# Performance work log

Hardware: AMD Instinct MI355X
Metric: run time of the kernel (lower is better)

Reference implementation:

```python
import jax, jax.numpy as jnp
import numpy as np
from jax.ops import segment_sum

NUM_GRAPHS = 1024

def setup_inputs() -> dict:
    key = jax.random.key(0)
    ks = jax.random.split(key, 10)
    N, E = 100000, 6400000
    x = jax.random.normal(ks[0], (N, 3), dtype=jnp.float32)
    edge_index = jax.random.randint(ks[1], (2, E), 0, N, dtype=jnp.int64)
    batch = jnp.sort(jax.random.randint(ks[2], (N,), 0, NUM_GRAPHS, dtype=jnp.int64))
    # GCNConv weights (glorot-ish scale) and biases
    W1 = jax.random.normal(ks[3], (3, 16), dtype=jnp.float32) * (1.0 / np.sqrt(3))
    b1 = jnp.zeros((16,), dtype=jnp.float32)
    W2 = jax.random.normal(ks[4], (16, 32), dtype=jnp.float32) * (1.0 / np.sqrt(16))
    b2 = jnp.zeros((32,), dtype=jnp.float32)
    Wl = jax.random.normal(ks[5], (32, 3), dtype=jnp.float32) * (1.0 / np.sqrt(32))
    bl = jnp.zeros((3,), dtype=jnp.float32)
    return {"x": x, "edge_index": edge_index, "batch": batch,
            "W1": W1, "b1": b1, "W2": W2, "b2": b2, "Wl": Wl, "bl": bl}

def _gcn_conv(x, src, dst, norm, W, b, num_nodes):
    # h = X W ; out[dst] += norm * h[src]  (symmetric-normalized scatter-add)
    h = x @ W                                    # [N, F_out]
    msg = h[src] * norm[:, None]                 # [E+N, F_out]
    out = segment_sum(msg, dst, num_segments=num_nodes)
    return out + b

def reference(x, edge_index, batch, W1, b1, W2, b2, Wl, bl):
    N = x.shape[0]
    # add self-loops (PyG GCNConv default)
    loops = jnp.arange(N, dtype=edge_index.dtype)
    src = jnp.concatenate([edge_index[0], loops])
    dst = jnp.concatenate([edge_index[1], loops])
    # symmetric normalization: deg over destination, norm = d^-1/2[src] * d^-1/2[dst]
    deg = segment_sum(jnp.ones_like(dst, dtype=x.dtype), dst, num_segments=N)
    dinv = jnp.where(deg > 0, jax.lax.rsqrt(deg), 0.0)
    norm = dinv[src] * dinv[dst]
    h = jax.nn.relu(_gcn_conv(x, src, dst, norm, W1, b1, N))
    h = jax.nn.relu(_gcn_conv(h, src, dst, norm, W2, b2, N))
    # global mean pool over graphs
    sums = segment_sum(h, batch, num_segments=NUM_GRAPHS)          # [G, 32]
    cnts = segment_sum(jnp.ones((N,), dtype=h.dtype), batch, num_segments=NUM_GRAPHS)
    pooled = sums / jnp.maximum(cnts, 1.0)[:, None]
    return pooled @ Wl + bl
```

## Files before the change

### kernel.cpp

```cpp
#include <hip/hip_runtime.h>
#include <hip/hip_fp16.h>

#define NG 1024
#define SCAN_B 1024
#define BSH2 9
#define GN 512
#define MAXBIN 256
#define NB2 256
#define SCB 1024
#define TSZ 8192
#define TS2 8192
#define PGR 64

__global__ void k_scanA(const int* __restrict__ in, int* __restrict__ tmp,
                        int* __restrict__ part, int L) {
    __shared__ int s[SCAN_B];
    int gid = blockIdx.x * SCAN_B + threadIdx.x;
    s[threadIdx.x] = (gid < L) ? in[gid] : 0;
    __syncthreads();
    for (int off = 1; off < SCAN_B; off <<= 1) {
        int t = (threadIdx.x >= off) ? s[threadIdx.x - off] : 0;
        __syncthreads();
        s[threadIdx.x] += t;
        __syncthreads();
    }
    if (gid < L) tmp[gid] = s[threadIdx.x];
    if (threadIdx.x == SCAN_B - 1) part[blockIdx.x] = s[SCAN_B - 1];
}

__global__ void k_scanB(int* __restrict__ part, int NB) {
    __shared__ int s[SCAN_B];
    int v = (threadIdx.x < NB) ? part[threadIdx.x] : 0;
    s[threadIdx.x] = v;
    __syncthreads();
    for (int off = 1; off < SCAN_B; off <<= 1) {
        int t = (threadIdx.x >= off) ? s[threadIdx.x - off] : 0;
        __syncthreads();
        s[threadIdx.x] += t;
        __syncthreads();
    }
    if (threadIdx.x < NB) part[threadIdx.x] = threadIdx.x ? s[threadIdx.x - 1] : 0;
}

__global__ void k_applyT(const int* __restrict__ tmp2, const int* __restrict__ part2,
                         int* __restrict__ histT, int L,
                         float* __restrict__ pooled, float* __restrict__ cnt) {
    int k = blockIdx.x * blockDim.x + threadIdx.x;
    if (k < L) {
        int incl = tmp2[k] + part2[k >> 10];
        int orig = histT[k];
        histT[k] = incl - orig;
        if (k == L - 1) histT[L] = incl;
    }
    if (k < NG * 32) pooled[k] = 0.0f;
    if (k < NG) cnt[k] = 0.0f;
}

__global__ __launch_bounds__(SCB) void k_hist(const int* __restrict__ dst,
                                              int* __restrict__ histT,
                                              int E, int CH, int NBIN) {
    __shared__ int cnt_s[MAXBIN];
    if (threadIdx.x < MAXBIN) cnt_s[threadIdx.x] = 0;
    __syncthreads();
    int blk = blockIdx.x;
    int s0 = blk * CH, s1 = s0 + CH; if (s1 > E) s1 = E;
    for (int e = s0 + threadIdx.x; e < s1; e += SCB)
        atomicAdd(&cnt_s[dst[e] >> BSH2], 1);
    __syncthreads();
    for (int b = threadIdx.x; b < NBIN; b += SCB)
        histT[b * NB2 + blk] = cnt_s[b];
}

__global__ __launch_bounds__(1024) void k_scatter(const int* __restrict__ src,
                                                  const int* __restrict__ dst,
                                                  const int* __restrict__ offT,
                                                  unsigned* __restrict__ binned,
                                                  int E, int CH, int NBIN) {
    __shared__ unsigned stg[TSZ];
    __shared__ unsigned char sbin[TSZ];
    __shared__ int th[MAXBIN];
    __shared__ int sc[MAXBIN];
    __shared__ int toff[MAXBIN + 1];
    __shared__ int gcur[MAXBIN];
    int tid = threadIdx.x;
    int blk = blockIdx.x;
    if (tid < MAXBIN) {
        th[tid] = 0;
        gcur[tid] = (tid < NBIN) ? offT[tid * NB2 + blk] : 0;
    }
    __syncthreads();
    int s0 = blk * CH, s1 = s0 + CH; if (s1 > E) s1 = E;
    for (int t0 = s0; t0 < s1; t0 += TSZ) {
        int cnt = s1 - t0; if (cnt > TSZ) cnt = TSZ;
        unsigned pk[8]; int rk[8]; int bn[8];
#pragma unroll
        for (int j = 0; j < 8; ++j) {
            int e = t0 + tid + j * 1024;
            bn[j] = -1;
            if (e < t0 + cnt) {
                int d = dst[e];
                int b = d >> BSH2;
                pk[j] = (unsigned)src[e] | ((unsigned)(d & (GN - 1)) << 17);
                bn[j] = b;
                rk[j] = atomicAdd(&th[b], 1);
            }
        }
        __syncthreads();
        if (tid < MAXBIN) sc[tid] = th[tid];
        __syncthreads();
        for (int off = 1; off < MAXBIN; off <<= 1) {
            int v = 0;
            if (tid < MAXBIN && tid >= off) v = sc[tid - off];
            __syncthreads();
            if (tid < MAXBIN) sc[tid] += v;
            __syncthreads();
        }
        if (tid < MAXBIN) toff[tid + 1] = sc[tid];
        if (tid == 0) toff[0] = 0;
        __syncthreads();
#pragma unroll
        for (int j = 0; j < 8; ++j)
            if (bn[j] >= 0) {
                int p = toff[bn[j]] + rk[j];
                stg[p] = pk[j];
                sbin[p] = (unsigned char)bn[j];
            }
        __syncthreads();
#pragma unroll 4
        for (int i = tid; i < cnt; i += 1024) {
            int b = sbin[i];
            binned[gcur[b] + (i - toff[b])] = stg[i];
        }
        __syncthreads();
        if (tid < MAXBIN) { gcur[tid] += th[tid]; th[tid] = 0; }
        __syncthreads();
    }
}

__global__ __launch_bounds__(1024) void k_csr4(
        const unsigned* __restrict__ binned, const int* __restrict__ offT,
        int* __restrict__ row_ptr, float* __restrict__ dinv,
        const float* __restrict__ x, float4* __restrict__ xd,
        int* __restrict__ csr, int N, int NBIN) {
    __shared__ unsigned stg[TS2];
    __shared__ unsigned short sdl[TS2];
    __shared__ int cnt[GN];
    __shared__ int pre[GN];
    __shared__ int run[GN];
    __shared__ int th[GN];
    __shared__ int toff[GN + 1];
    int tid = threadIdx.x;
    int b = blockIdx.x;
    int base = offT[b * NB2];
    int end  = offT[(b + 1) * NB2];
    if (tid < GN) cnt[tid] = 0;
    __syncthreads();
    for (int i = base + tid; i < end; i += 1024)
        atomicAdd(&cnt[(binned[i] >> 17) & (GN - 1)], 1);
    __syncthreads();
    if (tid < GN) pre[tid] = cnt[tid];
    __syncthreads();
    for (int off = 1; off < GN; off <<= 1) {
        int v = 0;
        if (tid < GN && tid >= off) v = pre[tid - off];
        __syncthreads();
        if (tid < GN) pre[tid] += v;
        __syncthreads();
    }
    int gv = (b << BSH2) + tid;
    if (tid < GN) {
        pre[tid] -= cnt[tid];
        run[tid] = 0;
        th[tid] = 0;
        if (gv < N) {
            row_ptr[gv] = base + pre[tid];
            float d = rsqrtf((float)cnt[tid] + 1.0f);
            dinv[gv] = d;
            xd[gv] = make_float4(d * x[gv * 3 + 0], d * x[gv * 3 + 1],
                                 d * x[gv * 3 + 2], 0.0f);
        }
    }
    if (b == NBIN - 1 && tid == 0) row_ptr[N] = end;
    __syncthreads();
    for (int t0 = base; t0 < end; t0 += TS2) {
        int tc = end - t0; if (tc > TS2) tc = TS2;
        unsigned pk[8]; int rk[8], dl[8];
#pragma unroll
        for (int j = 0; j < 8; ++j) {
            int e = t0 + tid + j * 1024;
            dl[j] = -1;
            if (e < t0 + tc) {
                unsigned p = binned[e];
                pk[j] = p;
                dl[j] = (int)((p >> 17) & (GN - 1));
                rk[j] = atomicAdd(&th[dl[j]], 1);
            }
        }
        __syncthreads();
        if (tid < GN) toff[tid + 1] = th[tid];
        if (tid == 0) toff[0] = 0;
        __syncthreads();
        for (int off = 1; off < GN; off <<= 1) {
            int v = 0;
            if (tid < GN && tid + 1 > off) v = toff[tid + 1 - off];
            __syncthreads();
            if (tid < GN) toff[tid + 1] += v;
            __syncthreads();
        }
#pragma unroll
        for (int j = 0; j < 8; ++j)
            if (dl[j] >= 0) {
                int p = toff[dl[j]] + rk[j];
                stg[p] = pk[j];
                sdl[p] = (unsigned short)dl[j];
            }
        __syncthreads();
#pragma unroll 4
        for (int i = tid; i < tc; i += 1024) {
            int d = sdl[i];
            csr[base + pre[d] + run[d] + (i - toff[d])] = (int)(stg[i] & 0x1FFFFu);
        }
        __syncthreads();
        if (tid < GN) { run[tid] += th[tid]; th[tid] = 0; }
        __syncthreads();
    }
}

__global__ __launch_bounds__(256) void k_ga(const int* __restrict__ row_ptr,
                                            const int* __restrict__ csr,
                                            const float4* __restrict__ xd,
                                            const float* __restrict__ dinv,
                                            const float* __restrict__ W1,
                                            const float* __restrict__ b1,
                                            __half* __restrict__ g1h, int N) {
    __shared__ float sW[48];
    __shared__ float sb[16];
    if (threadIdx.x < 48) sW[threadIdx.x] = W1[threadIdx.x];
    if (threadIdx.x < 16) sb[threadIdx.x] = b1[threadIdx.x];
    __syncthreads();
    int t = blockIdx.x * blockDim.x + threadIdx.x;
    int v = t >> 3, l = t & 7;
    if (v >= N) return;
    int beg = row_ptr[v], end = row_ptr[v + 1];
    float sx = 0.0f, sy = 0.0f, sz = 0.0f;
#pragma unroll 8
    for (int e = beg + l; e < end; e += 8) {
        float4 a = xd[csr[e]];
        sx += a.x; sy += a.y; sz += a.z;
    }
    sx += __shfl_xor(sx, 1, 64); sy += __shfl_xor(sy, 1, 64); sz += __shfl_xor(sz, 1, 64);
    sx += __shfl_xor(sx, 2, 64); sy += __shfl_xor(sy, 2, 64); sz += __shfl_xor(sz, 2, 64);
    sx += __shfl_xor(sx, 4, 64); sy += __shfl_xor(sy, 4, 64); sz += __shfl_xor(sz, 4, 64);
    float4 self = xd[v];
    sx += self.x; sy += self.y; sz += self.z;
    float d = dinv[v];
    int f0 = l * 2;
    float h0 = fmaxf(d * (sx * sW[f0]     + sy * sW[16 + f0]     + sz * sW[32 + f0])     + sb[f0],     0.0f);
    float h1 = fmaxf(d * (sx * sW[f0 + 1] + sy * sW[16 + f0 + 1] + sz * sW[32 + f0 + 1]) + sb[f0 + 1], 0.0f);
    __half2 p = __halves2half2(__float2half(d * h0), __float2half(d * h1));
    *(unsigned*)(g1h + (size_t)v * 16 + f0) = *(unsigned*)&p;
}

__global__ __launch_bounds__(256) void k_gb(const int* __restrict__ row_ptr,
                                            const int* __restrict__ csr,
                                            const __half* __restrict__ g1h,
                                            const float* __restrict__ dinv,
                                            const float* __restrict__ W2,
                                            const float* __restrict__ b2,
                                            const int* __restrict__ batch,
                                            float* __restrict__ pooled,
                                            float* __restrict__ cnt, int N) {
    __shared__ float sW[512];
    __shared__ float sb[32];
    __shared__ float sacc[PGR * 32];
    __shared__ int   scnt[PGR];
    __shared__ int   sgf;
    int t = threadIdx.x;
    for (int i = t; i < 512; i += 256) sW[i] = W2[i];
    if (t < 32) sb[t] = b2[t];
    for (int i = t; i < PGR * 32; i += 256) sacc[i] = 0.0f;
    if (t < PGR) scnt[t] = 0;
    int v0 = blockIdx.x * 32;
    if (t == 0) sgf = (v0 < N) ? batch[v0] : 0;
    __syncthreads();
    int gt = blockIdx.x * blockDim.x + t;
    int v = gt >> 3, l = gt & 7;
    int gfirst = sgf;
    if (v < N) {
        const uint4* g4 = (const uint4*)g1h;
        float s16[16];
#pragma unroll
        for (int j = 0; j < 16; ++j) s16[j] = 0.0f;
        int beg = row_ptr[v], end = row_ptr[v + 1];
#pragma unroll 4
        for (int e = beg + l; e < end; e += 8) {
            int s = csr[e];
            uint4 lo = g4[(size_t)s * 2];
            uint4 hi = g4[(size_t)s * 2 + 1];
            float2 f;
            f = __half22float2(*(__half2*)&lo.x); s16[0]  += f.x; s16[1]  += f.y;
            f = __half22float2(*(__half2*)&lo.y); s16[2]  += f.x; s16[3]  += f.y;
            f = __half22float2(*(__half2*)&lo.z); s16[4]  += f.x; s16[5]  += f.y;
            f = __half22float2(*(__half2*)&lo.w); s16[6]  += f.x; s16[7]  += f.y;
            f = __half22float2(*(__half2*)&hi.x); s16[8]  += f.x; s16[9]  += f.y;
            f = __half22float2(*(__half2*)&hi.y); s16[10] += f.x; s16[11] += f.y;
            f = __half22float2(*(__half2*)&hi.z); s16[12] += f.x; s16[13] += f.y;
            f = __half22float2(*(__half2*)&hi.w); s16[14] += f.x; s16[15] += f.y;
        }
        if (l == 0) {
            uint4 lo = g4[(size_t)v * 2];
            uint4 hi = g4[(size_t)v * 2 + 1];
            float2 f;
            f = __half22float2(*(__half2*)&lo.x); s16[0]  += f.x; s16[1]  += f.y;
            f = __half22float2(*(__half2*)&lo.y); s16[2]  += f.x; s16[3]  += f.y;
            f = __half22float2(*(__half2*)&lo.z); s16[4]  += f.x; s16[5]  += f.y;
            f = __half22float2(*(__half2*)&lo.w); s16[6]  += f.x; s16[7]  += f.y;
            f = __half22float2(*(__half2*)&hi.x); s16[8]  += f.x; s16[9]  += f.y;
            f = __half22float2(*(__half2*)&hi.y); s16[10] += f.x; s16[11] += f.y;
            f = __half22float2(*(__half2*)&hi.z); s16[12] += f.x; s16[13] += f.y;
            f = __half22float2(*(__half2*)&hi.w); s16[14] += f.x; s16[15] += f.y;
        }
#pragma unroll
        for (int j = 0; j < 16; ++j) {
            s16[j] += __shfl_xor(s16[j], 1, 64);
            s16[j] += __shfl_xor(s16[j], 2, 64);
            s16[j] += __shfl_xor(s16[j], 4, 64);
        }
        float d = dinv[v];
        int g = batch[v];
        int gl = g - gfirst;
        int f0 = l * 4;
#pragma unroll
        for (int j = 0; j < 4; ++j) {
            float acc = 0.0f;
#pragma unroll
            for (int k = 0; k < 16; ++k) acc += s16[k] * sW[k * 32 + f0 + j];
            float h = fmaxf(d * acc + sb[f0 + j], 0.0f);
            if (gl < PGR) atomicAdd(&sacc[gl * 32 + f0 + j], h);
            else          atomicAdd(&pooled[g * 32 + f0 + j], h);
        }
        if (l == 0) {
            if (gl < PGR) atomicAdd(&scnt[gl], 1);
            else          atomicAdd(&cnt[g], 1.0f);
        }
    }
    __syncthreads();
    for (int i = t; i < PGR * 32; i += 256) {
        float val = sacc[i];
        if (val != 0.0f) atomicAdd(&pooled[(gfirst + (i >> 5)) * 32 + (i & 31)], val);
    }
    for (int i = t; i < PGR; i += 256) {
        int c = scnt[i];
        if (c) atomicAdd(&cnt[gfirst + i], (float)c);
    }
}

__global__ void k_out(const float* __restrict__ pooled, const float* __restrict__ cnt,
                      const float* __restrict__ Wl, const float* __restrict__ bl,
                      float* __restrict__ out) {
    int t = blockIdx.x * blockDim.x + threadIdx.x;
    if (t >= NG * 3) return;
    int g = t / 3, c = t % 3;
    float inv = 1.0f / fmaxf(cnt[g], 1.0f);
    float s = bl[c];
#pragma unroll
    for (int f = 0; f < 32; ++f) s += pooled[g * 32 + f] * inv * Wl[f * 3 + c];
    out[g * 3 + c] = s;
}

extern "C" void kernel_launch(void* const* d_in, const int* in_sizes, int n_in,
                              void* d_out, int out_size, void* d_ws, size_t ws_size,
                              hipStream_t stream) {
    const float* x     = (const float*)d_in[0];
    const int*   ei    = (const int*)d_in[1];
    const int*   batch = (const int*)d_in[2];
    const float* W1    = (const float*)d_in[3];
    const float* b1    = (const float*)d_in[4];
    const float* W2    = (const float*)d_in[5];
    const float* b2    = (const float*)d_in[6];
    const float* Wl    = (const float*)d_in[7];
    const float* bl    = (const float*)d_in[8];

    const int N = in_sizes[0] / 3;
    const int E = in_sizes[1] / 2;
    const int* src = ei;
    const int* dst = ei + E;
    const int NBIN = (N + GN - 1) >> BSH2;
    const int CH   = (E + NB2 - 1) / NB2;
    const int L    = NBIN * NB2;

    char* w = (char*)d_ws;
    int*      row_ptr = (int*)w;      w += (size_t)(N + 4) * 4;
    float*    dinv    = (float*)w;    w += (size_t)N * 4;
    int*      histT   = (int*)w;      w += (size_t)(L + 4) * 4;
    int*      tmp2    = (int*)w;      w += (size_t)L * 4;
    int*      part2   = (int*)w;      w += (size_t)SCAN_B * 4;
    unsigned* binned  = (unsigned*)w; w += (size_t)(E + 16) * 4;
    int*      csr     = (int*)w;      w += (size_t)E * 4;
    float4*   xd      = (float4*)w;   w += (size_t)N * 16;
    __half*   g1h     = (__half*)w;   w += ((size_t)N * 32 + 15) & ~(size_t)15;
    float*    pooled  = (float*)w;    w += (size_t)NG * 32 * 4;
    float*    cnt     = (float*)w;    w += (size_t)NG * 4;

    const int B = 256;
    const int NBl = (L + SCAN_B - 1) / SCAN_B;

    k_hist<<<NB2, SCB, 0, stream>>>(dst, histT, E, CH, NBIN);
    k_scanA<<<NBl, SCAN_B, 0, stream>>>(histT, tmp2, part2, L);
    k_scanB<<<1, SCAN_B, 0, stream>>>(part2, NBl);
    k_applyT<<<(L + B - 1) / B, B, 0, stream>>>(tmp2, part2, histT, L, pooled, cnt);
    k_scatter<<<NB2, 1024, 0, stream>>>(src, dst, histT, binned, E, CH, NBIN);
    k_csr4<<<NBIN, 1024, 0, stream>>>(binned, histT, row_ptr, dinv, x, xd, csr, N, NBIN);

    k_ga<<<((size_t)N * 8 + B - 1) / B, B, 0, stream>>>(row_ptr, csr, xd, dinv, W1, b1, g1h, N);
    k_gb<<<((size_t)N * 8 + B - 1) / B, B, 0, stream>>>(row_ptr, csr, g1h, dinv, W2, b2, batch,
                                                        pooled, cnt, N);
    k_out<<<(NG * 3 + B - 1) / B, B, 0, stream>>>(pooled, cnt, Wl, bl, (float*)d_out);
}
```

Measured before the change: 175.4 us.

## Fuse layer-1 aggregation into CSR build via LDS atomics, split degree pass

The CSR build kernel is split in two. The first pass computes degrees, row_ptr, dinv and the pre-scaled features xd. The second pass builds the CSR and, while streaming the binned edges, gathers xd[src] and accumulates it per destination with shared-memory float atomics. It then computes the layer-1 output directly, which removes the separate k_ga kernel and its second read of the CSR. This adds an extra pass over the binned edges to count degrees. It also adds LDS float atomic contention and gives up the 8-lanes-per-node layout for the final per-node transform.

```diff
diff --git a/kernel.cpp b/kernel.cpp
--- a/kernel.cpp
+++ b/kernel.cpp
@@ -137,18 +137,12 @@
     }
 }
 
-__global__ __launch_bounds__(1024) void k_csr4(
+__global__ __launch_bounds__(1024) void k_csr4a(
         const unsigned* __restrict__ binned, const int* __restrict__ offT,
         int* __restrict__ row_ptr, float* __restrict__ dinv,
-        const float* __restrict__ x, float4* __restrict__ xd,
-        int* __restrict__ csr, int N, int NBIN) {
-    __shared__ unsigned stg[TS2];
-    __shared__ unsigned short sdl[TS2];
+        const float* __restrict__ x, float4* __restrict__ xd, int N, int NBIN) {
     __shared__ int cnt[GN];
     __shared__ int pre[GN];
-    __shared__ int run[GN];
-    __shared__ int th[GN];
-    __shared__ int toff[GN + 1];
     int tid = threadIdx.x;
     int b = blockIdx.x;
     int base = offT[b * NB2];
@@ -168,23 +162,49 @@
         __syncthreads();
     }
     int gv = (b << BSH2) + tid;
+    if (tid < GN && gv < N) {
+        row_ptr[gv] = base + pre[tid] - cnt[tid];
+        float d = rsqrtf((float)cnt[tid] + 1.0f);
+        dinv[gv] = d;
+        xd[gv] = make_float4(d * x[gv * 3 + 0], d * x[gv * 3 + 1],
+                             d * x[gv * 3 + 2], 0.0f);
+    }
+    if (b == NBIN - 1 && tid == 0) row_ptr[N] = end;
+}
+
+__global__ __launch_bounds__(1024) void k_csr4b(
+        const unsigned* __restrict__ binned, const int* __restrict__ offT,
+        const int* __restrict__ row_ptr, const float* __restrict__ dinv,
+        const float4* __restrict__ xd, const float* __restrict__ W1,
+        const float* __restrict__ b1, int* __restrict__ csr,
+        __half* __restrict__ g1h, int N, int NBIN) {
+    __shared__ unsigned stg[TS2];
+    __shared__ int rp[GN];
+    __shared__ int run[GN];
+    __shared__ int th[GN];
+    __shared__ int toff[GN + 1];
+    __shared__ float xax[GN];
+    __shared__ float xay[GN];
+    __shared__ float xaz[GN];
+    __shared__ float sW[48];
+    __shared__ float sb[16];
+    int tid = threadIdx.x;
+    int b = blockIdx.x;
+    int base = offT[b * NB2];
+    int end  = offT[(b + 1) * NB2];
+    int first = b << BSH2;
+    if (tid < 48) sW[tid] = W1[tid];
+    if (tid < 16) sb[tid] = b1[tid];
     if (tid < GN) {
-        pre[tid] -= cnt[tid];
-        run[tid] = 0;
-        th[tid] = 0;
-        if (gv < N) {
-            row_ptr[gv] = base + pre[tid];
-            float d = rsqrtf((float)cnt[tid] + 1.0f);
-            dinv[gv] = d;
-            xd[gv] = make_float4(d * x[gv * 3 + 0], d * x[gv * 3 + 1],
-                                 d * x[gv * 3 + 2], 0.0f);
-        }
-    }
-    if (b == NBIN - 1 && tid == 0) row_ptr[N] = end;
+        int gv = first + tid;
+        rp[tid] = (gv < N) ? row_ptr[gv] : end;
+        run[tid] = 0; th[tid] = 0;
+        xax[tid] = 0.0f; xay[tid] = 0.0f; xaz[tid] = 0.0f;
+    }
     __syncthreads();
     for (int t0 = base; t0 < end; t0 += TS2) {
         int tc = end - t0; if (tc > TS2) tc = TS2;
-        unsigned pk[8]; int rk[8], dl[8];
+        unsigned pk[8]; int rk[8], dl[8]; float4 xs[8];
 #pragma unroll
         for (int j = 0; j < 8; ++j) {
             int e = t0 + tid + j * 1024;
@@ -194,8 +214,16 @@
                 pk[j] = p;
                 dl[j] = (int)((p >> 17) & (GN - 1));
                 rk[j] = atomicAdd(&th[dl[j]], 1);
+                xs[j] = xd[p & 0x1FFFFu];
             }
         }
+#pragma unroll
+        for (int j = 0; j < 8; ++j)
+            if (dl[j] >= 0) {
+                atomicAdd(&xax[dl[j]], xs[j].x);
+                atomicAdd(&xay[dl[j]], xs[j].y);
+                atomicAdd(&xaz[dl[j]], xs[j].z);
+            }
         __syncthreads();
         if (tid < GN) toff[tid + 1] = th[tid];
         if (tid == 0) toff[0] = 0;
@@ -209,56 +237,35 @@
         }
 #pragma unroll
         for (int j = 0; j < 8; ++j)
-            if (dl[j] >= 0) {
-                int p = toff[dl[j]] + rk[j];
-                stg[p] = pk[j];
-                sdl[p] = (unsigned short)dl[j];
-            }
+            if (dl[j] >= 0) stg[toff[dl[j]] + rk[j]] = pk[j];
         __syncthreads();
 #pragma unroll 4
         for (int i = tid; i < tc; i += 1024) {
-            int d = sdl[i];
-            csr[base + pre[d] + run[d] + (i - toff[d])] = (int)(stg[i] & 0x1FFFFu);
+            unsigned p = stg[i];
+            int d = (int)((p >> 17) & (GN - 1));
+            csr[rp[d] + run[d] + (i - toff[d])] = (int)(p & 0x1FFFFu);
         }
         __syncthreads();
         if (tid < GN) { run[tid] += th[tid]; th[tid] = 0; }
         __syncthreads();
     }
-}
-
-__global__ __launch_bounds__(256) void k_ga(const int* __restrict__ row_ptr,
-                                            const int* __restrict__ csr,
-                                            const float4* __restrict__ xd,
-                                            const float* __restrict__ dinv,
-                                            const float* __restrict__ W1,
-                                            const float* __restrict__ b1,
-                                            __half* __restrict__ g1h, int N) {
-    __shared__ float sW[48];
-    __shared__ float sb[16];
-    if (threadIdx.x < 48) sW[threadIdx.x] = W1[threadIdx.x];
-    if (threadIdx.x < 16) sb[threadIdx.x] = b1[threadIdx.x];
-    __syncthreads();
-    int t = blockIdx.x * blockDim.x + threadIdx.x;
-    int v = t >> 3, l = t & 7;
-    if (v >= N) return;
-    int beg = row_ptr[v], end = row_ptr[v + 1];
-    float sx = 0.0f, sy = 0.0f, sz = 0.0f;
-#pragma unroll 8
-    for (int e = beg + l; e < end; e += 8) {
-        float4 a = xd[csr[e]];
-        sx += a.x; sy += a.y; sz += a.z;
-    }
-    sx += __shfl_xor(sx, 1, 64); sy += __shfl_xor(sy, 1, 64); sz += __shfl_xor(sz, 1, 64);
-    sx += __shfl_xor(sx, 2, 64); sy += __shfl_xor(sy, 2, 64); sz += __shfl_xor(sz, 2, 64);
-    sx += __shfl_xor(sx, 4, 64); sy += __shfl_xor(sy, 4, 64); sz += __shfl_xor(sz, 4, 64);
-    float4 self = xd[v];
-    sx += self.x; sy += self.y; sz += self.z;
-    float d = dinv[v];
-    int f0 = l * 2;
-    float h0 = fmaxf(d * (sx * sW[f0]     + sy * sW[16 + f0]     + sz * sW[32 + f0])     + sb[f0],     0.0f);
-    float h1 = fmaxf(d * (sx * sW[f0 + 1] + sy * sW[16 + f0 + 1] + sz * sW[32 + f0 + 1]) + sb[f0 + 1], 0.0f);
-    __half2 p = __halves2half2(__float2half(d * h0), __float2half(d * h1));
-    *(unsigned*)(g1h + (size_t)v * 16 + f0) = *(unsigned*)&p;
+    if (tid < GN) {
+        int gv = first + tid;
+        if (gv < N) {
+            float4 self = xd[gv];
+            float sx = xax[tid] + self.x;
+            float sy = xay[tid] + self.y;
+            float sz = xaz[tid] + self.z;
+            float d = dinv[gv];
+#pragma unroll
+            for (int f0 = 0; f0 < 16; f0 += 2) {
+                float h0 = fmaxf(d * (sx * sW[f0]     + sy * sW[16 + f0]     + sz * sW[32 + f0])     + sb[f0],     0.0f);
+                float h1 = fmaxf(d * (sx * sW[f0 + 1] + sy * sW[16 + f0 + 1] + sz * sW[32 + f0 + 1]) + sb[f0 + 1], 0.0f);
+                __half2 p = __halves2half2(__float2half(d * h0), __float2half(d * h1));
+                *(unsigned*)(g1h + (size_t)gv * 16 + f0) = *(unsigned*)&p;
+            }
+        }
+    }
 }
 
 __global__ __launch_bounds__(256) void k_gb(const int* __restrict__ row_ptr,
@@ -410,9 +417,9 @@
     k_scanB<<<1, SCAN_B, 0, stream>>>(part2, NBl);
     k_applyT<<<(L + B - 1) / B, B, 0, stream>>>(tmp2, part2, histT, L, pooled, cnt);
     k_scatter<<<NB2, 1024, 0, stream>>>(src, dst, histT, binned, E, CH, NBIN);
-    k_csr4<<<NBIN, 1024, 0, stream>>>(binned, histT, row_ptr, dinv, x, xd, csr, N, NBIN);
-
-    k_ga<<<((size_t)N * 8 + B - 1) / B, B, 0, stream>>>(row_ptr, csr, xd, dinv, W1, b1, g1h, N);
+    k_csr4a<<<NBIN, 1024, 0, stream>>>(binned, histT, row_ptr, dinv, x, xd, N, NBIN);
+    k_csr4b<<<NBIN, 1024, 0, stream>>>(binned, histT, row_ptr, dinv, xd, W1, b1,
+                                       csr, g1h, N, NBIN);
     k_gb<<<((size_t)N * 8 + B - 1) / B, B, 0, stream>>>(row_ptr, csr, g1h, dinv, W2, b2, batch,
                                                         pooled, cnt, N);
     k_out<<<(NG * 3 + B - 1) / B, B, 0, stream>>>(pooled, cnt, Wl, bl, (float*)d_out);
```

Result: slower. 289.4 us (+65.0%).
